# Kernel optimization log

Measured on AMD Instinct MI355X. Metric: run time of the kernel, lower is better.

## Reference

```python
import jax, jax.numpy as jnp
import numpy as np

H, DH = 8, 64  # num_heads, head_dim


def setup_inputs() -> dict:
    key = jax.random.key(0)
    ks = jax.random.split(key, 7)
    m, nq, nkv, d = 4, 2048, 2048, 512
    return {
        "xq": jax.random.normal(ks[0], (m, nq, d), jnp.float32),
        "xk": jax.random.normal(ks[1], (m, nkv, d), jnp.float32),
        "xv": jax.random.normal(ks[2], (m, nkv, d), jnp.float32),
        "Wq": jax.random.normal(ks[3], (d, H * DH), jnp.float32) * 0.02,
        "Wk": jax.random.normal(ks[4], (d, H * DH), jnp.float32) * 0.02,
        "Wv": jax.random.normal(ks[5], (d, H * DH), jnp.float32) * 0.02,
        "Wo": jax.random.normal(ks[6], (H * DH, d), jnp.float32) * 0.02,
        "bo": jnp.zeros((d,), jnp.float32),
    }


def _split_heads(t):
    # [b, n, h*d] -> [b, h, n, d]
    b, n, _ = t.shape
    return t.reshape(b, n, H, DH).transpose(0, 2, 1, 3)


def reference(xq, xk, xv, Wq, Wk, Wv, Wo, bo):
    scale = DH ** -0.5
    q = _split_heads(xq @ Wq)   # [b,h,nq,dh]
    k = _split_heads(xk @ Wk)   # [b,h,nkv,dh]
    v = _split_heads(xv @ Wv)   # [b,h,nkv,dh]
    dots = jnp.einsum("bhqd,bhkd->bhqk", q, k) * scale  # [b,h,nq,nkv]
    # diagonal attention term: query attends to its own (k,v) projection
    xq_k = _split_heads(xq @ Wk)
    xq_v = _split_heads(xq @ Wv)
    diag = jnp.sum(q * xq_k, axis=-1, keepdims=True) * scale  # [b,h,nq,1]
    dots = jnp.concatenate([dots, diag], axis=-1)  # [b,h,nq,nkv+1]
    attn = jax.nn.softmax(dots, axis=-1)
    out = jnp.einsum("bhqk,bhkd->bhqd", attn[..., :-1], v) + attn[..., -1:] * xq_v
    b, _, nq, _ = out.shape
    out = out.transpose(0, 2, 1, 3).reshape(b, nq, H * DH)  # merge heads
    return out @ Wo + bo
```

## Files before the change

### kernel.cpp

```cpp
#include <hip/hip_runtime.h>

#define LOG2E 1.44269504088896f
#define CS (0.125f * LOG2E)

typedef __bf16 bf16x8 __attribute__((ext_vector_type(8)));
typedef float f32x4 __attribute__((ext_vector_type(4)));
typedef unsigned short u16x8 __attribute__((ext_vector_type(8)));

__device__ __forceinline__ unsigned short f2bf(float f) {
  union { float f; unsigned int u; } v{f};
  unsigned int r = v.u + 0x7fffu + ((v.u >> 16) & 1u);
  return (unsigned short)(r >> 16);
}
__device__ __forceinline__ float bf2f(unsigned short u) {
  union { unsigned int u; float f; } v; v.u = ((unsigned int)u) << 16; return v.f;
}
__device__ __forceinline__ unsigned int pkr(float a, float b) {
  unsigned int ua = __builtin_bit_cast(unsigned int, a) + 0x8000u;
  unsigned int ub = __builtin_bit_cast(unsigned int, b) + 0x8000u;
  return __builtin_amdgcn_perm(ub, ua, 0x07060302);
}

typedef __attribute__((address_space(3))) unsigned int lds32_t;
typedef const __attribute__((address_space(1))) unsigned int glb32_t;
__device__ __forceinline__ void gld16(const unsigned short* g, unsigned short* l) {
  __builtin_amdgcn_global_load_lds((glb32_t*)(unsigned long long)g,
                                   (lds32_t*)(unsigned int)(unsigned long long)l,
                                   16, 0, 0);
}

__global__ __launch_bounds__(256) void conv_x(
    const float* __restrict__ xq, const float* __restrict__ xk, const float* __restrict__ xv,
    unsigned short* __restrict__ oq, unsigned short* __restrict__ ok, unsigned short* __restrict__ ov) {
  const int N4 = (8192 * 512) / 4;
  int idx = blockIdx.x * 256 + threadIdx.x;
  const float* src; unsigned short* dst; int i;
  if (idx < N4)          { src = xq; dst = oq; i = idx; }
  else if (idx < 2 * N4) { src = xk; dst = ok; i = idx - N4; }
  else                   { src = xv; dst = ov; i = idx - 2 * N4; }
  float4 v = ((const float4*)src)[i];
  ushort4 o; o.x = f2bf(v.x); o.y = f2bf(v.y); o.z = f2bf(v.z); o.w = f2bf(v.w);
  ((ushort4*)dst)[i] = o;
}

__global__ __launch_bounds__(256) void conv_w(
    const float* __restrict__ Wq, const float* __restrict__ Wk,
    const float* __restrict__ Wv, const float* __restrict__ Wo,
    unsigned short* __restrict__ oWq, unsigned short* __restrict__ oWk,
    unsigned short* __restrict__ oWv, unsigned short* __restrict__ oWo) {
  __shared__ unsigned short T[64 * 65];
  const int wsel = blockIdx.x >> 6;
  const int tile = blockIdx.x & 63;
  const int tk = (tile >> 3) * 64, tn = (tile & 7) * 64;
  const float* src = (wsel == 0) ? Wq : (wsel == 1) ? Wk : (wsel == 2) ? Wv : Wo;
  unsigned short* dst = (wsel == 0) ? oWq : (wsel == 1) ? oWk : (wsel == 2) ? oWv : oWo;
  const float scale = (wsel == 0) ? CS : 1.0f;
  const int rr = threadIdx.x >> 4;
  const int cc = (threadIdx.x & 15) * 4;
#pragma unroll
  for (int i = 0; i < 4; i++) {
    int row = rr + i * 16;
    float4 v = *(const float4*)&src[(size_t)(tk + row) * 512 + tn + cc];
    T[(cc + 0) * 65 + row] = f2bf(v.x * scale);
    T[(cc + 1) * 65 + row] = f2bf(v.y * scale);
    T[(cc + 2) * 65 + row] = f2bf(v.z * scale);
    T[(cc + 3) * 65 + row] = f2bf(v.w * scale);
  }
  __syncthreads();
#pragma unroll
  for (int i = 0; i < 4; i++) {
    int n = rr + i * 16;
    ushort4 o;
    o.x = T[n * 65 + cc + 0]; o.y = T[n * 65 + cc + 1];
    o.z = T[n * 65 + cc + 2]; o.w = T[n * 65 + cc + 3];
    *(ushort4*)&dst[(size_t)(tn + n) * 512 + tk + cc] = o;
  }
}

__device__ __forceinline__ void gemm_tile(
    const unsigned short* __restrict__ A, const unsigned short* __restrict__ Bt,
    int rowBlk, int colBlk, unsigned short* As, unsigned short* Bs, f32x4 (&acc)[4][4]) {
  const int t = threadIdx.x;
  const int lane = t & 63, c = lane & 15, g = lane >> 4;
  const int w = t >> 6;
  const int wm = w & 1, wn = w >> 1;
#pragma unroll
  for (int i = 0; i < 4; i++)
#pragma unroll
    for (int j = 0; j < 4; j++)
#pragma unroll
      for (int r = 0; r < 4; r++) acc[i][j][r] = 0.f;

  for (int kk = 0; kk < 512; kk += 32) {
    __syncthreads();
#pragma unroll
    for (int i = 0; i < 2; i++) {
      int idx = t + 256 * i;
      int r = idx >> 2, ch = idx & 3;
      gld16(&A[(size_t)(rowBlk + r) * 512 + kk + ch * 8], &As[idx * 8]);
      gld16(&Bt[(size_t)(colBlk + r) * 512 + kk + ch * 8], &Bs[idx * 8]);
    }
    __syncthreads();
    bf16x8 af[4], bfr[4];
#pragma unroll
    for (int i = 0; i < 4; i++)
      af[i] = __builtin_bit_cast(bf16x8, *(const u16x8*)&As[(wm * 64 + i * 16 + c) * 32 + g * 8]);
#pragma unroll
    for (int j = 0; j < 4; j++)
      bfr[j] = __builtin_bit_cast(bf16x8, *(const u16x8*)&Bs[(wn * 64 + j * 16 + c) * 32 + g * 8]);
#pragma unroll
    for (int i = 0; i < 4; i++)
#pragma unroll
      for (int j = 0; j < 4; j++)
        acc[i][j] = __builtin_amdgcn_mfma_f32_16x16x32_bf16(af[i], bfr[j], acc[i][j], 0, 0, 0);
  }
}

__global__ __launch_bounds__(256) void proj_all(
    const unsigned short* __restrict__ xq, const unsigned short* __restrict__ xk,
    const unsigned short* __restrict__ xv,
    const unsigned short* __restrict__ Wq, const unsigned short* __restrict__ Wk,
    const unsigned short* __restrict__ Wv,
    unsigned short* __restrict__ Qo, unsigned short* __restrict__ XKo,
    unsigned short* __restrict__ XVo, unsigned short* __restrict__ Ko,
    unsigned short* __restrict__ Vto) {
  __shared__ unsigned short As[128 * 32];
  __shared__ unsigned short Bs[128 * 32];
  const int rowBlk = blockIdx.x * 128;
  const int y = blockIdx.y;
  const unsigned short* A; const unsigned short* Bt; int colBlk; int mode;
  unsigned short* out;
  if (y < 12) {
    int wsel = y >> 2;
    A = xq; colBlk = (y & 3) * 128; mode = 0;
    Bt = (wsel == 0) ? Wq : (wsel == 1) ? Wk : Wv;
    out = (wsel == 0) ? Qo : (wsel == 1) ? XKo : XVo;
  } else if (y < 16) {
    A = xk; Bt = Wk; out = Ko; colBlk = (y - 12) * 128; mode = 0;
  } else {
    A = xv; Bt = Wv; out = Vto; colBlk = (y - 16) * 128; mode = 1;
  }
  f32x4 acc[4][4];
  gemm_tile(A, Bt, rowBlk, colBlk, As, Bs, acc);
  const int t = threadIdx.x;
  const int w = t >> 6, lane = t & 63, c = lane & 15, g = lane >> 4;
  const int wm = w & 1, wn = w >> 1;
  if (mode == 0) {
#pragma unroll
    for (int i = 0; i < 4; i++)
#pragma unroll
      for (int j = 0; j < 4; j++)
#pragma unroll
        for (int r = 0; r < 4; r++) {
          int row = rowBlk + wm * 64 + i * 16 + g * 4 + r;
          int col = colBlk + wn * 64 + j * 16 + c;
          out[(size_t)row * 512 + col] = f2bf(acc[i][j][r]);
        }
  } else {
#pragma unroll
    for (int i = 0; i < 4; i++)
#pragma unroll
      for (int j = 0; j < 4; j++)
#pragma unroll
        for (int r = 0; r < 4; r++) {
          int row = rowBlk + wm * 64 + i * 16 + g * 4 + r;
          int col = colBlk + wn * 64 + j * 16 + c;
          int bb = row >> 11, n = row & 2047;
          int hh = col >> 6, dh = col & 63;
          out[((size_t)(bb * 8 + hh) * 64 + dh) * 2048 + n] = f2bf(acc[i][j][r]);
        }
  }
}

__global__ __launch_bounds__(256) void gemm_out(
    const unsigned short* __restrict__ A, const unsigned short* __restrict__ Bt,
    float* __restrict__ out, const float* __restrict__ bias) {
  __shared__ unsigned short As[128 * 32];
  __shared__ unsigned short Bs[128 * 32];
  const int rowBlk = blockIdx.x * 128;
  const int colBlk = blockIdx.y * 128;
  f32x4 acc[4][4];
  gemm_tile(A, Bt, rowBlk, colBlk, As, Bs, acc);
  const int t = threadIdx.x;
  const int w = t >> 6, lane = t & 63, c = lane & 15, g = lane >> 4;
  const int wm = w & 1, wn = w >> 1;
#pragma unroll
  for (int i = 0; i < 4; i++)
#pragma unroll
    for (int j = 0; j < 4; j++)
#pragma unroll
      for (int r = 0; r < 4; r++) {
        int row = rowBlk + wm * 64 + i * 16 + g * 4 + r;
        int col = colBlk + wn * 64 + j * 16 + c;
        out[(size_t)row * 512 + col] = acc[i][j][r] + bias[col];
      }
}

__global__ __launch_bounds__(512, 8) void attn_kernel(
    const unsigned short* __restrict__ Q, const unsigned short* __restrict__ K,
    const unsigned short* __restrict__ Vt, const unsigned short* __restrict__ XK,
    const unsigned short* __restrict__ XV, unsigned short* __restrict__ O) {
  __shared__ unsigned short Ks[64 * 72];
  __shared__ unsigned short Vs[64 * 72];
  __shared__ unsigned short Ps[8][16 * 72];
  __shared__ float Scr[8][32];
  const int t = threadIdx.x;
  const int w = t >> 6, lane = t & 63, c = lane & 15, g = lane >> 4;
  const int qt = blockIdx.x, h = blockIdx.y, b = blockIdx.z;
  const size_t hb = (size_t)b * (2048 * 512) + h * 64;
  const size_t vhb = (size_t)(b * 8 + h) * 64 * 2048;
  const int qbase = qt * 128 + w * 16;
  unsigned short* Pw = &Ps[w][0];

  const int sr = t >> 3, sch = t & 7;
  const size_t kgoff = hb + (size_t)sr * 512 + sch * 8;
  const size_t vgoff = vhb + (size_t)sr * 2048 + sch * 8;
  const int soff = sr * 72 + sch * 8;

  bf16x8 qf[2];
#pragma unroll
  for (int hf = 0; hf < 2; hf++)
    qf[hf] = __builtin_bit_cast(bf16x8,
        *(const u16x8*)&Q[hb + (size_t)(qbase + c) * 512 + hf * 32 + g * 8]);

  f32x4 accO[4];
  float lq = 0.f;
#pragma unroll
  for (int jd = 0; jd < 4; jd++)
#pragma unroll
    for (int r = 0; r < 4; r++) accO[jd][r] = 0.f;

  u16x8 kreg = *(const u16x8*)&K[kgoff];
  u16x8 vreg = *(const u16x8*)&Vt[vgoff];
  *(u16x8*)&Ks[soff] = kreg;
  *(u16x8*)&Vs[soff] = vreg;
  __syncthreads();

  for (int kt = 0; kt < 32; kt++) {
    if (kt < 31) {
      kreg = *(const u16x8*)&K[kgoff + (size_t)(kt + 1) * 64 * 512];
      vreg = *(const u16x8*)&Vt[vgoff + (size_t)(kt + 1) * 64];
    }

    f32x4 s[4];
#pragma unroll
    for (int j = 0; j < 4; j++) {
      bf16x8 kf0 = __builtin_bit_cast(bf16x8, *(const u16x8*)&Ks[(j * 16 + c) * 72 + g * 8]);
      bf16x8 kf1 = __builtin_bit_cast(bf16x8, *(const u16x8*)&Ks[(j * 16 + c) * 72 + 32 + g * 8]);
      f32x4 z; z[0] = z[1] = z[2] = z[3] = 0.f;
      z = __builtin_amdgcn_mfma_f32_16x16x32_bf16(kf0, qf[0], z, 0, 0, 0);
      z = __builtin_amdgcn_mfma_f32_16x16x32_bf16(kf1, qf[1], z, 0, 0, 0);
      s[j] = z;
    }

    float sum = 0.f;
#pragma unroll
    for (int j = 0; j < 4; j++) {
      float p0 = exp2f(s[j][0]);
      float p1 = exp2f(s[j][1]);
      float p2 = exp2f(s[j][2]);
      float p3 = exp2f(s[j][3]);
      sum += (p0 + p1) + (p2 + p3);
      uint2 pw; pw.x = pkr(p0, p1); pw.y = pkr(p2, p3);
      *(uint2*)&Pw[c * 72 + j * 16 + g * 4] = pw;
    }
    lq += sum;

    bf16x8 pf0 = __builtin_bit_cast(bf16x8, *(const u16x8*)&Pw[c * 72 + g * 8]);
    bf16x8 pf1 = __builtin_bit_cast(bf16x8, *(const u16x8*)&Pw[c * 72 + 32 + g * 8]);
#pragma unroll
    for (int jd = 0; jd < 4; jd++) {
      bf16x8 v0 = __builtin_bit_cast(bf16x8, *(const u16x8*)&Vs[(jd * 16 + c) * 72 + g * 8]);
      bf16x8 v1 = __builtin_bit_cast(bf16x8, *(const u16x8*)&Vs[(jd * 16 + c) * 72 + 32 + g * 8]);
      accO[jd] = __builtin_amdgcn_mfma_f32_16x16x32_bf16(pf0, v0, accO[jd], 0, 0, 0);
      accO[jd] = __builtin_amdgcn_mfma_f32_16x16x32_bf16(pf1, v1, accO[jd], 0, 0, 0);
    }

    if (kt < 31) {
      __syncthreads();
      *(u16x8*)&Ks[soff] = kreg;
      *(u16x8*)&Vs[soff] = vreg;
      __syncthreads();
    }
  }

  lq += __shfl_xor(lq, 16);
  lq += __shfl_xor(lq, 32);

  {
    const int qc = qbase + c;
    float part = 0.f;
    {
      const unsigned short* qp = &Q[hb + (size_t)qc * 512 + g * 16];
      const unsigned short* xp = &XK[hb + (size_t)qc * 512 + g * 16];
      u16x8 q0 = *(const u16x8*)&qp[0], q1 = *(const u16x8*)&qp[8];
      u16x8 x0 = *(const u16x8*)&xp[0], x1 = *(const u16x8*)&xp[8];
#pragma unroll
      for (int ii = 0; ii < 8; ii++)
        part += bf2f(q0[ii]) * bf2f(x0[ii]) + bf2f(q1[ii]) * bf2f(x1[ii]);
    }
    part += __shfl_xor(part, 16);
    part += __shfl_xor(part, 32);
    float pd = exp2f(part);
    float inv = 1.f / (lq + pd);
    if (g == 0) {
      Scr[w][c] = inv;
      Scr[w][16 + c] = pd * inv;
    }
    __builtin_amdgcn_s_waitcnt(0);
    f32x4 a4 = *(const f32x4*)&Scr[w][g * 4];
    f32x4 p4 = *(const f32x4*)&Scr[w][16 + g * 4];
#pragma unroll
    for (int jd = 0; jd < 4; jd++)
#pragma unroll
      for (int r = 0; r < 4; r++) {
        int qr = qbase + g * 4 + r;
        float xv = bf2f(XV[hb + (size_t)qr * 512 + jd * 16 + c]);
        float val = accO[jd][r] * a4[r] + p4[r] * xv;
        O[((size_t)(b * 2048 + qr)) * 512 + h * 64 + jd * 16 + c] = f2bf(val);
      }
  }
}

extern "C" void kernel_launch(void* const* d_in, const int* in_sizes, int n_in,
                              void* d_out, int out_size, void* d_ws, size_t ws_size,
                              hipStream_t stream) {
  const float* xq = (const float*)d_in[0];
  const float* xk = (const float*)d_in[1];
  const float* xv = (const float*)d_in[2];
  const float* Wq = (const float*)d_in[3];
  const float* Wk = (const float*)d_in[4];
  const float* Wv = (const float*)d_in[5];
  const float* Wo = (const float*)d_in[6];
  const float* bo = (const float*)d_in[7];

  unsigned short* ws = (unsigned short*)d_ws;
  const size_t MD = 8192ull * 512;
  const size_t WD = 512ull * 512;
  unsigned short* xq_b = ws;
  unsigned short* xk_b = xq_b + MD;
  unsigned short* xv_b = xk_b + MD;
  unsigned short* Wq_t = xv_b + MD;
  unsigned short* Wk_t = Wq_t + WD;
  unsigned short* Wv_t = Wk_t + WD;
  unsigned short* Wo_t = Wv_t + WD;
  unsigned short* Qb  = Wo_t + WD;
  unsigned short* Kb  = Qb + MD;
  unsigned short* Vtb = Kb + MD;
  unsigned short* XKb = Vtb + MD;
  unsigned short* XVb = XKb + MD;
  unsigned short* Ob  = XVb + MD;

  conv_x<<<dim3(12288), 256, 0, stream>>>(xq, xk, xv, xq_b, xk_b, xv_b);
  conv_w<<<dim3(256), 256, 0, stream>>>(Wq, Wk, Wv, Wo, Wq_t, Wk_t, Wv_t, Wo_t);
  proj_all<<<dim3(64, 20), 256, 0, stream>>>(xq_b, xk_b, xv_b, Wq_t, Wk_t, Wv_t,
                                             Qb, XKb, XVb, Kb, Vtb);
  attn_kernel<<<dim3(16, 8, 4), 512, 0, stream>>>(Qb, Kb, Vtb, XKb, XVb, Ob);
  gemm_out<<<dim3(64, 4), 256, 0, stream>>>(Ob, Wo_t, (float*)d_out, bo);
}
```

Measured before the change: 229.3 us.

## Load K/V fragments directly from global in attention and merge conversion kernels

The attention kernel drops its LDS staging of K and V tiles and the double __syncthreads per iteration. Each wave now loads its MFMA operand fragments straight from global memory, relying on L2/cache reuse across the 8 waves that share the same K/V. It also fuses the x and weight conversion kernels into one launch and lowers the occupancy hint in launch_bounds from 8 to 4. The risk is more global/L2 traffic and exposed load latency, since there is no explicit prefetch and each wave re-reads K/V independently.

```diff
diff --git a/kernel.cpp b/kernel.cpp
--- a/kernel.cpp
+++ b/kernel.cpp
@@ -29,51 +29,53 @@
                                    16, 0, 0);
 }
 
-__global__ __launch_bounds__(256) void conv_x(
+__global__ __launch_bounds__(256) void conv_all(
     const float* __restrict__ xq, const float* __restrict__ xk, const float* __restrict__ xv,
-    unsigned short* __restrict__ oq, unsigned short* __restrict__ ok, unsigned short* __restrict__ ov) {
-  const int N4 = (8192 * 512) / 4;
-  int idx = blockIdx.x * 256 + threadIdx.x;
-  const float* src; unsigned short* dst; int i;
-  if (idx < N4)          { src = xq; dst = oq; i = idx; }
-  else if (idx < 2 * N4) { src = xk; dst = ok; i = idx - N4; }
-  else                   { src = xv; dst = ov; i = idx - 2 * N4; }
-  float4 v = ((const float4*)src)[i];
-  ushort4 o; o.x = f2bf(v.x); o.y = f2bf(v.y); o.z = f2bf(v.z); o.w = f2bf(v.w);
-  ((ushort4*)dst)[i] = o;
-}
-
-__global__ __launch_bounds__(256) void conv_w(
     const float* __restrict__ Wq, const float* __restrict__ Wk,
     const float* __restrict__ Wv, const float* __restrict__ Wo,
+    unsigned short* __restrict__ oxq, unsigned short* __restrict__ oxk, unsigned short* __restrict__ oxv,
     unsigned short* __restrict__ oWq, unsigned short* __restrict__ oWk,
     unsigned short* __restrict__ oWv, unsigned short* __restrict__ oWo) {
   __shared__ unsigned short T[64 * 65];
-  const int wsel = blockIdx.x >> 6;
-  const int tile = blockIdx.x & 63;
-  const int tk = (tile >> 3) * 64, tn = (tile & 7) * 64;
-  const float* src = (wsel == 0) ? Wq : (wsel == 1) ? Wk : (wsel == 2) ? Wv : Wo;
-  unsigned short* dst = (wsel == 0) ? oWq : (wsel == 1) ? oWk : (wsel == 2) ? oWv : oWo;
-  const float scale = (wsel == 0) ? CS : 1.0f;
-  const int rr = threadIdx.x >> 4;
-  const int cc = (threadIdx.x & 15) * 4;
-#pragma unroll
-  for (int i = 0; i < 4; i++) {
-    int row = rr + i * 16;
-    float4 v = *(const float4*)&src[(size_t)(tk + row) * 512 + tn + cc];
-    T[(cc + 0) * 65 + row] = f2bf(v.x * scale);
-    T[(cc + 1) * 65 + row] = f2bf(v.y * scale);
-    T[(cc + 2) * 65 + row] = f2bf(v.z * scale);
-    T[(cc + 3) * 65 + row] = f2bf(v.w * scale);
-  }
-  __syncthreads();
-#pragma unroll
-  for (int i = 0; i < 4; i++) {
-    int n = rr + i * 16;
-    ushort4 o;
-    o.x = T[n * 65 + cc + 0]; o.y = T[n * 65 + cc + 1];
-    o.z = T[n * 65 + cc + 2]; o.w = T[n * 65 + cc + 3];
-    *(ushort4*)&dst[(size_t)(tn + n) * 512 + tk + cc] = o;
+  const int blk = blockIdx.x;
+  if (blk < 12288) {
+    const int N4 = (8192 * 512) / 4;
+    int idx = blk * 256 + threadIdx.x;
+    const float* src; unsigned short* dst; int i;
+    if (idx < N4)          { src = xq; dst = oxq; i = idx; }
+    else if (idx < 2 * N4) { src = xk; dst = oxk; i = idx - N4; }
+    else                   { src = xv; dst = oxv; i = idx - 2 * N4; }
+    float4 v = ((const float4*)src)[i];
+    ushort4 o; o.x = f2bf(v.x); o.y = f2bf(v.y); o.z = f2bf(v.z); o.w = f2bf(v.w);
+    ((ushort4*)dst)[i] = o;
+  } else {
+    const int wblk = blk - 12288;
+    const int wsel = wblk >> 6;
+    const int tile = wblk & 63;
+    const int tk = (tile >> 3) * 64, tn = (tile & 7) * 64;
+    const float* src = (wsel == 0) ? Wq : (wsel == 1) ? Wk : (wsel == 2) ? Wv : Wo;
+    unsigned short* dst = (wsel == 0) ? oWq : (wsel == 1) ? oWk : (wsel == 2) ? oWv : oWo;
+    const float scale = (wsel == 0) ? CS : 1.0f;
+    const int rr = threadIdx.x >> 4;
+    const int cc = (threadIdx.x & 15) * 4;
+#pragma unroll
+    for (int i = 0; i < 4; i++) {
+      int row = rr + i * 16;
+      float4 v = *(const float4*)&src[(size_t)(tk + row) * 512 + tn + cc];
+      T[(cc + 0) * 65 + row] = f2bf(v.x * scale);
+      T[(cc + 1) * 65 + row] = f2bf(v.y * scale);
+      T[(cc + 2) * 65 + row] = f2bf(v.z * scale);
+      T[(cc + 3) * 65 + row] = f2bf(v.w * scale);
+    }
+    __syncthreads();
+#pragma unroll
+    for (int i = 0; i < 4; i++) {
+      int n = rr + i * 16;
+      ushort4 o;
+      o.x = T[n * 65 + cc + 0]; o.y = T[n * 65 + cc + 1];
+      o.z = T[n * 65 + cc + 2]; o.w = T[n * 65 + cc + 3];
+      *(ushort4*)&dst[(size_t)(tn + n) * 512 + tk + cc] = o;
+    }
   }
 }
 
@@ -196,12 +198,10 @@
       }
 }
 
-__global__ __launch_bounds__(512, 8) void attn_kernel(
+__global__ __launch_bounds__(512, 4) void attn_kernel(
     const unsigned short* __restrict__ Q, const unsigned short* __restrict__ K,
     const unsigned short* __restrict__ Vt, const unsigned short* __restrict__ XK,
     const unsigned short* __restrict__ XV, unsigned short* __restrict__ O) {
-  __shared__ unsigned short Ks[64 * 72];
-  __shared__ unsigned short Vs[64 * 72];
   __shared__ unsigned short Ps[8][16 * 72];
   __shared__ float Scr[8][32];
   const int t = threadIdx.x;
@@ -212,11 +212,6 @@
   const int qbase = qt * 128 + w * 16;
   unsigned short* Pw = &Ps[w][0];
 
-  const int sr = t >> 3, sch = t & 7;
-  const size_t kgoff = hb + (size_t)sr * 512 + sch * 8;
-  const size_t vgoff = vhb + (size_t)sr * 2048 + sch * 8;
-  const int soff = sr * 72 + sch * 8;
-
   bf16x8 qf[2];
 #pragma unroll
   for (int hf = 0; hf < 2; hf++)
@@ -230,26 +225,26 @@
 #pragma unroll
     for (int r = 0; r < 4; r++) accO[jd][r] = 0.f;
 
-  u16x8 kreg = *(const u16x8*)&K[kgoff];
-  u16x8 vreg = *(const u16x8*)&Vt[vgoff];
-  *(u16x8*)&Ks[soff] = kreg;
-  *(u16x8*)&Vs[soff] = vreg;
-  __syncthreads();
+  const unsigned short* Kp = &K[hb + (size_t)c * 512 + g * 8];
+  const unsigned short* Vp = &Vt[vhb + (size_t)c * 2048 + g * 8];
 
   for (int kt = 0; kt < 32; kt++) {
-    if (kt < 31) {
-      kreg = *(const u16x8*)&K[kgoff + (size_t)(kt + 1) * 64 * 512];
-      vreg = *(const u16x8*)&Vt[vgoff + (size_t)(kt + 1) * 64];
+    const int kb = kt * 64;
+
+    bf16x8 kf0[4], kf1[4];
+#pragma unroll
+    for (int j = 0; j < 4; j++) {
+      const unsigned short* kr = Kp + (size_t)(kb + j * 16) * 512;
+      kf0[j] = __builtin_bit_cast(bf16x8, *(const u16x8*)kr);
+      kf1[j] = __builtin_bit_cast(bf16x8, *(const u16x8*)(kr + 32));
     }
 
     f32x4 s[4];
 #pragma unroll
     for (int j = 0; j < 4; j++) {
-      bf16x8 kf0 = __builtin_bit_cast(bf16x8, *(const u16x8*)&Ks[(j * 16 + c) * 72 + g * 8]);
-      bf16x8 kf1 = __builtin_bit_cast(bf16x8, *(const u16x8*)&Ks[(j * 16 + c) * 72 + 32 + g * 8]);
       f32x4 z; z[0] = z[1] = z[2] = z[3] = 0.f;
-      z = __builtin_amdgcn_mfma_f32_16x16x32_bf16(kf0, qf[0], z, 0, 0, 0);
-      z = __builtin_amdgcn_mfma_f32_16x16x32_bf16(kf1, qf[1], z, 0, 0, 0);
+      z = __builtin_amdgcn_mfma_f32_16x16x32_bf16(kf0[j], qf[0], z, 0, 0, 0);
+      z = __builtin_amdgcn_mfma_f32_16x16x32_bf16(kf1[j], qf[1], z, 0, 0, 0);
       s[j] = z;
     }
 
@@ -270,18 +265,14 @@
     bf16x8 pf1 = __builtin_bit_cast(bf16x8, *(const u16x8*)&Pw[c * 72 + 32 + g * 8]);
 #pragma unroll
     for (int jd = 0; jd < 4; jd++) {
-      bf16x8 v0 = __builtin_bit_cast(bf16x8, *(const u16x8*)&Vs[(jd * 16 + c) * 72 + g * 8]);
-      bf16x8 v1 = __builtin_bit_cast(bf16x8, *(const u16x8*)&Vs[(jd * 16 + c) * 72 + 32 + g * 8]);
+      const unsigned short* vr = Vp + (size_t)(jd * 16) * 2048 + kb;
+      bf16x8 v0 = __builtin_bit_cast(bf16x8, *(const u16x8*)vr);
+      bf16x8 v1 = __builtin_bit_cast(bf16x8, *(const u16x8*)(vr + 32));
       accO[jd] = __builtin_amdgcn_mfma_f32_16x16x32_bf16(pf0, v0, accO[jd], 0, 0, 0);
       accO[jd] = __builtin_amdgcn_mfma_f32_16x16x32_bf16(pf1, v1, accO[jd], 0, 0, 0);
     }
 
-    if (kt < 31) {
-      __syncthreads();
-      *(u16x8*)&Ks[soff] = kreg;
-      *(u16x8*)&Vs[soff] = vreg;
-      __syncthreads();
-    }
+    __builtin_amdgcn_s_barrier();
   }
 
   lq += __shfl_xor(lq, 16);
@@ -351,8 +342,8 @@
   unsigned short* XVb = XKb + MD;
   unsigned short* Ob  = XVb + MD;
 
-  conv_x<<<dim3(12288), 256, 0, stream>>>(xq, xk, xv, xq_b, xk_b, xv_b);
-  conv_w<<<dim3(256), 256, 0, stream>>>(Wq, Wk, Wv, Wo, Wq_t, Wk_t, Wv_t, Wo_t);
+  conv_all<<<dim3(12544), 256, 0, stream>>>(xq, xk, xv, Wq, Wk, Wv, Wo,
+                                            xq_b, xk_b, xv_b, Wq_t, Wk_t, Wv_t, Wo_t);
   proj_all<<<dim3(64, 20), 256, 0, stream>>>(xq_b, xk_b, xv_b, Wq_t, Wk_t, Wv_t,
                                              Qb, XKb, XVb, Kb, Vtb);
   attn_kernel<<<dim3(16, 8, 4), 512, 0, stream>>>(Qb, Kb, Vtb, XKb, XVb, Ob);
```

After: 387.0 us. +68.8%, slower.
